# Optimization experiments

Measured on AMD Instinct MI355X. Metric: run time of the kernel, lower is better.

The kernel has to match this reference:

```python
import jax, jax.numpy as jnp
import numpy as np

E_LAMBDA = 1e-4


def _conv1d(x, w, b=None, pad=0):
    # x: (C, L) unbatched, w: (O, I, K)
    y = jax.lax.conv_general_dilated(
        x[None], w, window_strides=(1,), padding=[(pad, pad)],
        dimension_numbers=("NCH", "OIH", "NCH"))[0]
    if b is not None:
        y = y + b[:, None]
    return y


def _avg_pool2(x):
    # kernel 2 stride 2 along last axis; x: (C, L) -> (C, L//2)
    C, L = x.shape
    return x.reshape(C, L // 2, 2).mean(axis=-1)


def _simam(x):
    # x: (C, L); torch version runs on (1, C, L) so stats are global
    n = x.shape[0] * x.shape[1] - 1
    d = (x - x.mean()) ** 2
    y = d / (4.0 * (d.sum() / n + E_LAMBDA)) + 0.5
    return x + x * jax.nn.sigmoid(y)


def setup_inputs() -> dict:
    key = jax.random.key(0)
    ks = jax.random.split(key, 6)
    C, L = 2048, 4096  # L must equal 2*C for Tiss broadcast to be valid
    inp = jax.random.normal(ks[0], (C, L), dtype=jnp.float32)
    insum = jax.random.normal(ks[1], (C, L), dtype=jnp.float32)
    conv1_w = jax.random.normal(ks[2], (C, C, 3), dtype=jnp.float32) * (1.0 / np.sqrt(3 * C))
    fc_w = jax.random.normal(ks[3], (C, C, 1), dtype=jnp.float32) * (1.0 / np.sqrt(C))
    fc_b = jax.random.normal(ks[4], (C,), dtype=jnp.float32) * 0.01
    mix_w = jnp.array([-0.8], dtype=jnp.float32)
    return {"input": inp, "insum": insum, "conv1_w": conv1_w,
            "fc_w": fc_w, "fc_b": fc_b, "mix_w": mix_w}


def reference(input, insum, conv1_w, fc_w, fc_b, mix_w):
    x = _avg_pool2(input)        # (C, L/2)
    x_mfcc = _avg_pool2(insum)   # (C, L/2)

    input_new = _simam(input)
    insum_new = _simam(insum)

    x1 = _conv1d(x, conv1_w, pad=1)          # (C, L/2)
    x_mfcc1 = _conv1d(x_mfcc, conv1_w, pad=1)
    x2 = _conv1d(x, fc_w, fc_b, pad=0).T      # (L/2, C)
    x_mfcc2 = _conv1d(x_mfcc1, fc_w, fc_b, pad=0).T  # (L/2, C)

    out1 = jax.nn.sigmoid((x1 @ x_mfcc2).sum(axis=1))          # (C,)
    out2 = jax.nn.sigmoid((x_mfcc1.T @ x2.T).sum(axis=1))      # (L/2,) == (C,)

    mf = jax.nn.sigmoid(mix_w)                                  # (1,)
    out = out1 * mf + out2 * (1.0 - mf)                         # (C,)

    out = jax.nn.sigmoid(_conv1d(out[:, None], conv1_w, pad=1))  # (C, 1)

    input_insum = input_new * 0.6 + insum_new * 0.4             # (C, L)
    return input_insum * out
```

## Files before the change

### kernel.cpp

```cpp
#include <hip/hip_runtime.h>
#include <math.h>

#define C  2048
#define L  4096
#define L2 2048
#define CW3 6144

constexpr size_t OFF_RS_A = 0;
constexpr size_t OFF_RQ_A = 2048;
constexpr size_t OFF_RS_B = 4096;
constexpr size_t OFF_RQ_B = 6144;
constexpr size_t OFF_SCAL = 8192;
constexpr size_t OFF_CW   = 8208;
constexpr size_t OFF_G    = 10256;
constexpr size_t OFF_H    = 16400;
constexpr size_t OFF_V    = 22544;
constexpr size_t OFF_O2   = 24592;
constexpr size_t OFF_S    = 26640;
constexpr size_t OFF_U    = 28688;
constexpr size_t OFF_MIX  = 34832;

constexpr size_t PA_OFF = 0;
constexpr size_t PB_OFF = 4194304;

__device__ __forceinline__ float wredf(float v) {
#pragma unroll
  for (int o = 32; o; o >>= 1) v += __shfl_down(v, o, 64);
  return v;
}
__device__ __forceinline__ double wredd(double v) {
#pragma unroll
  for (int o = 32; o; o >>= 1) v += __shfl_down(v, o, 64);
  return v;
}
__device__ __forceinline__ float sigm(float x) { return 1.f / (1.f + expf(-x)); }
__device__ __forceinline__ float simam1(float x, float m, float cf) {
  float d = x - m;
  float y = d * d * cf + 0.5f;
  return x * (1.f + 1.f / (1.f + expf(-y)));
}

__global__ void w1(const float* __restrict__ A, const float* __restrict__ B,
                   const float* __restrict__ fc_w, float* __restrict__ ws,
                   float* __restrict__ dout) {
  int u = blockIdx.x;
  int tid = threadIdx.x;
  if (u < 4096) {
    __shared__ float sm[8];
    const float* src = (u < 2048) ? A : B;
    int row = u & 2047;
    const float4* p = (const float4*)(src + (size_t)row * L);
    float2* pool = (float2*)(dout + ((u < 2048) ? PA_OFF : PB_OFF) + (size_t)row * L2);
    float s = 0.f, q = 0.f;
#pragma unroll
    for (int i = tid; i < L / 4; i += 256) {
      float4 v = p[i];
      s += (v.x + v.y) + (v.z + v.w);
      q += (v.x * v.x + v.y * v.y) + (v.z * v.z + v.w * v.w);
      float2 pm;
      pm.x = (v.x + v.y) * 0.5f;
      pm.y = (v.z + v.w) * 0.5f;
      pool[i] = pm;
    }
    s = wredf(s); q = wredf(q);
    int lane = tid & 63, wv = tid >> 6;
    if (!lane) { sm[wv] = s; sm[4 + wv] = q; }
    __syncthreads();
    if (!tid) {
      float* rs = ws + ((u < 2048) ? OFF_RS_A : OFF_RS_B);
      float* rq = ws + ((u < 2048) ? OFF_RQ_A : OFF_RQ_B);
      rs[row] = sm[0] + sm[1] + sm[2] + sm[3];
      rq[row] = sm[4] + sm[5] + sm[6] + sm[7];
    }
  } else {
    int cb = u - 4096;
    int rg = cb >> 3;
    int col = (cb & 7) * 256 + tid;
    const float* p = fc_w + (size_t)rg * 64 * C + col;
    float acc = 0.f;
#pragma unroll 8
    for (int k = 0; k < 64; ++k) acc += p[(size_t)k * C];
    atomicAdd(ws + OFF_CW + col, acc);
  }
}

__global__ void w2(const float* __restrict__ fc_w, const float* __restrict__ fc_b,
                   float* __restrict__ ws) {
  int u = blockIdx.x;
  int tid = threadIdx.x;
  int lane = tid & 63, wv = tid >> 6;
  if (u < 2048) {
    __shared__ float sl[4];
    const float4* w = (const float4*)(fc_w + (size_t)u * C);
    const float4* rx = (const float4*)(ws + OFF_RS_A);
    float acc = 0.f;
#pragma unroll
    for (int i = tid; i < C / 4; i += 256) {
      float4 a = w[i], r = rx[i];
      acc += a.x * r.x + a.y * r.y + a.z * r.z + a.w * r.w;
    }
    acc = wredf(acc);
    if (!lane) sl[wv] = acc;
    __syncthreads();
    if (!tid)
      (ws + OFF_S)[u] = 0.5f * (sl[0] + sl[1] + sl[2] + sl[3]) + (float)L2 * fc_b[u];
  } else {
    __shared__ double sd[5];
    const float* arr = ws + (wv == 0 ? OFF_RS_A : wv == 1 ? OFF_RQ_A
                                                          : wv == 2 ? OFF_RS_B : OFF_RQ_B);
    double acc = 0.0, accb = 0.0;
    for (int i = lane; i < 2048; i += 64) {
      acc += (double)arr[i];
      if (wv == 0) accb += (double)fc_b[i];
    }
    acc = wredd(acc);
    if (wv == 0) accb = wredd(accb);
    if (!lane) { sd[wv] = acc; if (wv == 0) sd[4] = accb; }
    __syncthreads();
    if (!tid) {
      const double N = (double)C * (double)L, n = N - 1.0;
      double dA = sd[1] - sd[0] * sd[0] / N;
      double dB = sd[3] - sd[2] * sd[2] / N;
      float* s = ws + OFF_SCAL;
      s[0] = (float)(sd[0] / N);
      s[1] = (float)(1.0 / (4.0 * (dA / n + 1e-4)));
      s[2] = (float)(sd[2] / N);
      s[3] = (float)(1.0 / (4.0 * (dB / n + 1e-4)));
      s[4] = (float)sd[4];
    }
  }
}

__global__ void w3(const float* __restrict__ conv1_w, float* __restrict__ ws) {
  __shared__ float lcw[64], ls[64];
  int u = blockIdx.x;
  int tid = threadIdx.x;
  int cc = u % 24, rg = u / 24;
  int col = cc * 256 + tid;
  int i0 = rg * 64;
  if (tid < 64) {
    lcw[tid] = (ws + OFF_CW)[i0 + tid];
    ls[tid] = (ws + OFF_S)[i0 + tid];
  }
  __syncthreads();
  const float* base = conv1_w + (size_t)i0 * CW3 + col;
  float ag = 0.f, ah = 0.f;
#pragma unroll 8
  for (int k = 0; k < 64; ++k) {
    float wv = base[(size_t)k * CW3];
    ag += lcw[k] * wv;
    ah += ls[k] * wv;
  }
  atomicAdd(ws + OFF_G + col, ag);
  atomicAdd(ws + OFF_H + col, ah);
}

__global__ void w4(const float* __restrict__ dout, float* __restrict__ ws) {
  __shared__ float gsh[48], hsh[48];
  int u = blockIdx.x;
  int tid = threadIdx.x;
  int kb = u & 7, cg = u >> 3;
  int c0 = cg * 16;
  int k = kb * 256 + tid;
  if (tid < 48) gsh[tid] = (ws + OFF_G)[c0 * 3 + tid];
  else if (tid >= 64 && tid < 112) hsh[tid - 64] = (ws + OFF_H)[c0 * 3 + tid - 64];
  __syncthreads();
  float accv = 0.f, acco = 0.f;
#pragma unroll
  for (int c = 0; c < 16; ++c) {
    const float* row = dout + PB_OFF + (size_t)(c0 + c) * L2;
    float xc = row[k];
    float xl = (k > 0) ? row[k - 1] : 0.f;
    float xr = (k < L2 - 1) ? row[k + 1] : 0.f;
    accv += gsh[c * 3] * xl + gsh[c * 3 + 1] * xc + gsh[c * 3 + 2] * xr;
    acco += hsh[c * 3] * xl + hsh[c * 3 + 1] * xc + hsh[c * 3 + 2] * xr;
  }
  atomicAdd(ws + OFF_V + k, accv);
  atomicAdd(ws + OFF_O2 + k, acco);
}

__global__ void w5(const float* __restrict__ dout, float* __restrict__ ws) {
  __shared__ float vsh[2050];
  __shared__ float s12[12];
  int u = blockIdx.x;
  int tid = threadIdx.x;
  float sb = (ws + OFF_SCAL)[4];
  if (tid == 0) { vsh[0] = 0.f; vsh[2049] = 0.f; }
  for (int j = tid; j < L2; j += 256) vsh[1 + j] = (ws + OFF_V)[j] + sb;
  __syncthreads();
  const float* prow = dout + PA_OFF + (size_t)u * L2;
  float a0 = 0.f, a1 = 0.f, a2 = 0.f;
#pragma unroll
  for (int j = tid; j < L2; j += 256) {
    float xm = prow[j];
    a0 += xm * vsh[j + 2];
    a1 += xm * vsh[j + 1];
    a2 += xm * vsh[j];
  }
  a0 = wredf(a0); a1 = wredf(a1); a2 = wredf(a2);
  int lane = tid & 63, wv = tid >> 6;
  if (!lane) { s12[wv] = a0; s12[4 + wv] = a1; s12[8 + wv] = a2; }
  __syncthreads();
  if (!tid) {
    (ws + OFF_U)[u * 3 + 0] = s12[0] + s12[1] + s12[2] + s12[3];
    (ws + OFF_U)[u * 3 + 1] = s12[4] + s12[5] + s12[6] + s12[7];
    (ws + OFF_U)[u * 3 + 2] = s12[8] + s12[9] + s12[10] + s12[11];
  }
}

__global__ void w6(const float* __restrict__ conv1_w, const float* __restrict__ mix_w,
                   float* __restrict__ ws) {
  __shared__ float sl[4];
  int u = blockIdx.x;
  int tid = threadIdx.x;
  const float4* w4p = (const float4*)(conv1_w + (size_t)u * CW3);
  const float4* u4 = (const float4*)(ws + OFF_U);
  float acc = 0.f;
#pragma unroll
  for (int m = tid; m < CW3 / 4; m += 256) {
    float4 wv = w4p[m], uv = u4[m];
    acc += wv.x * uv.x + wv.y * uv.y + wv.z * uv.z + wv.w * uv.w;
  }
  acc = wredf(acc);
  int lane = tid & 63, wv = tid >> 6;
  if (!lane) sl[wv] = acc;
  __syncthreads();
  if (!tid) {
    float mfv = sigm(mix_w[0]);
    float o1 = sigm(sl[0] + sl[1] + sl[2] + sl[3]);
    float o2 = sigm((ws + OFF_O2)[u]);
    (ws + OFF_MIX)[u] = o1 * mfv + o2 * (1.f - mfv);
  }
}

__global__ void w7(const float* __restrict__ input, const float* __restrict__ insum,
                   const float* __restrict__ conv1_w, float* __restrict__ out,
                   const float* __restrict__ ws) {
  __shared__ float sl[4];
  __shared__ float shov;
  int u = blockIdx.x;
  int tid = threadIdx.x;
  const float4* w4p = (const float4*)(conv1_w + (size_t)u * CW3);
  const float4* m4 = (const float4*)(ws + OFF_MIX);
  float acc = 0.f;
#pragma unroll
  for (int p = tid; p < 512; p += 256) {
    float4 f0 = w4p[3 * p], f1 = w4p[3 * p + 1], f2 = w4p[3 * p + 2];
    float4 m = m4[p];
    acc += f0.y * m.x + f1.x * m.y + f1.w * m.z + f2.z * m.w;
  }
  acc = wredf(acc);
  int lane = tid & 63, wv = tid >> 6;
  if (!lane) sl[wv] = acc;
  __syncthreads();
  if (!tid) shov = sigm(sl[0] + sl[1] + sl[2] + sl[3]);
  __syncthreads();
  float ovc = shov;
  const float* scal = ws + OFF_SCAL;
  float mA = scal[0], cA = scal[1], mB = scal[2], cB = scal[3];
  size_t base = (size_t)u * L;
  const float4* pa = (const float4*)(input + base);
  const float4* pb = (const float4*)(insum + base);
  float4* po = (float4*)(out + base);
#pragma unroll
  for (int i = tid; i < L / 4; i += 256) {
    float4 a = pa[i], b = pb[i], r;
    r.x = (simam1(a.x, mA, cA) * 0.6f + simam1(b.x, mB, cB) * 0.4f) * ovc;
    r.y = (simam1(a.y, mA, cA) * 0.6f + simam1(b.y, mB, cB) * 0.4f) * ovc;
    r.z = (simam1(a.z, mA, cA) * 0.6f + simam1(b.z, mB, cB) * 0.4f) * ovc;
    r.w = (simam1(a.w, mA, cA) * 0.6f + simam1(b.w, mB, cB) * 0.4f) * ovc;
    po[i] = r;
  }
}

extern "C" void kernel_launch(void* const* d_in, const int* in_sizes, int n_in,
                              void* d_out, int out_size, void* d_ws, size_t ws_size,
                              hipStream_t stream) {
  const float* input   = (const float*)d_in[0];
  const float* insum   = (const float*)d_in[1];
  const float* conv1_w = (const float*)d_in[2];
  const float* fc_w    = (const float*)d_in[3];
  const float* fc_b    = (const float*)d_in[4];
  const float* mix_w   = (const float*)d_in[5];
  float* out = (float*)d_out;
  float* ws  = (float*)d_ws;

  hipMemsetAsync((char*)d_ws + OFF_CW * 4, 0, 18432 * 4, stream);

  dim3 b(256);
  w1<<<4352, b, 0, stream>>>(input, insum, fc_w, ws, out);
  w2<<<2049, b, 0, stream>>>(fc_w, fc_b, ws);
  w3<<<768, b, 0, stream>>>(conv1_w, ws);
  w4<<<1024, b, 0, stream>>>(out, ws);
  w5<<<2048, b, 0, stream>>>(out, ws);
  w6<<<2048, b, 0, stream>>>(conv1_w, mix_w, ws);
  w7<<<2048, b, 0, stream>>>(input, insum, conv1_w, out, ws);
}
```

Baseline: 235.0 us.

## Fuse all stages into one cooperative persistent kernel and recompute pooling on the fly

Merges the seven separate kernels into a single cooperative kernel that uses grid-wide syncs between stages and grid-stride loops over the original block indices. The intent is to remove launch overheads and gaps between kernels. It also stops writing the pooled intermediates to the output buffer and instead recomputes the avg-pool from the raw input and insum rows in the later stages, which drops a write and reread of that data. The costs are the grid.sync barriers, a fixed persistent grid size, and extra reads of the full-resolution rows in the stencil stage.

```diff
diff --git a/kernel.cpp b/kernel.cpp
--- a/kernel.cpp
+++ b/kernel.cpp
@@ -1,5 +1,8 @@
 #include <hip/hip_runtime.h>
+#include <hip/hip_cooperative_groups.h>
 #include <math.h>
+
+namespace cg = cooperative_groups;
 
 #define C  2048
 #define L  4096
@@ -20,9 +23,6 @@
 constexpr size_t OFF_U    = 28688;
 constexpr size_t OFF_MIX  = 34832;
 
-constexpr size_t PA_OFF = 0;
-constexpr size_t PB_OFF = 4194304;
-
 __device__ __forceinline__ float wredf(float v) {
 #pragma unroll
   for (int o = 32; o; o >>= 1) v += __shfl_down(v, o, 64);
@@ -40,236 +40,234 @@
   return x * (1.f + 1.f / (1.f + expf(-y)));
 }
 
-__global__ void w1(const float* __restrict__ A, const float* __restrict__ B,
-                   const float* __restrict__ fc_w, float* __restrict__ ws,
-                   float* __restrict__ dout) {
-  int u = blockIdx.x;
-  int tid = threadIdx.x;
-  if (u < 4096) {
-    __shared__ float sm[8];
-    const float* src = (u < 2048) ? A : B;
-    int row = u & 2047;
-    const float4* p = (const float4*)(src + (size_t)row * L);
-    float2* pool = (float2*)(dout + ((u < 2048) ? PA_OFF : PB_OFF) + (size_t)row * L2);
-    float s = 0.f, q = 0.f;
+__global__ __launch_bounds__(256, 4) void fused(
+    const float* __restrict__ input, const float* __restrict__ insum,
+    const float* __restrict__ conv1_w, const float* __restrict__ fc_w,
+    const float* __restrict__ fc_b, const float* __restrict__ mix_w,
+    float* __restrict__ out, float* __restrict__ ws) {
+  cg::grid_group grid = cg::this_grid();
+  const int tid = threadIdx.x;
+  const int lane = tid & 63, wv = tid >> 6;
+  const int nb = gridDim.x;
+  __shared__ float smem[2064];
+  __shared__ double sdsh[5];
+
+  for (int u = blockIdx.x; u < 4352; u += nb) {
+    if (u < 4096) {
+      const float* src = (u < 2048) ? input : insum;
+      int row = u & 2047;
+      const float4* p = (const float4*)(src + (size_t)row * L);
+      float s = 0.f, q = 0.f;
+#pragma unroll
+      for (int i = tid; i < L / 4; i += 256) {
+        float4 v = p[i];
+        s += (v.x + v.y) + (v.z + v.w);
+        q += (v.x * v.x + v.y * v.y) + (v.z * v.z + v.w * v.w);
+      }
+      s = wredf(s); q = wredf(q);
+      if (!lane) { smem[wv] = s; smem[4 + wv] = q; }
+      __syncthreads();
+      if (!tid) {
+        float* rs = ws + ((u < 2048) ? OFF_RS_A : OFF_RS_B);
+        float* rq = ws + ((u < 2048) ? OFF_RQ_A : OFF_RQ_B);
+        rs[row] = smem[0] + smem[1] + smem[2] + smem[3];
+        rq[row] = smem[4] + smem[5] + smem[6] + smem[7];
+      }
+      __syncthreads();
+    } else {
+      int cb = u - 4096;
+      int rg = cb >> 3;
+      int col = (cb & 7) * 256 + tid;
+      const float* p = fc_w + (size_t)rg * 64 * C + col;
+      float acc = 0.f;
+#pragma unroll 8
+      for (int k = 0; k < 64; ++k) acc += p[(size_t)k * C];
+      atomicAdd(ws + OFF_CW + col, acc);
+    }
+  }
+  grid.sync();
+
+  for (int u = blockIdx.x; u < 2049; u += nb) {
+    if (u < 2048) {
+      const float4* w = (const float4*)(fc_w + (size_t)u * C);
+      const float4* rx = (const float4*)(ws + OFF_RS_A);
+      float acc = 0.f;
+#pragma unroll
+      for (int i = tid; i < C / 4; i += 256) {
+        float4 a = w[i], r = rx[i];
+        acc += a.x * r.x + a.y * r.y + a.z * r.z + a.w * r.w;
+      }
+      acc = wredf(acc);
+      if (!lane) smem[wv] = acc;
+      __syncthreads();
+      if (!tid)
+        (ws + OFF_S)[u] = 0.5f * (smem[0] + smem[1] + smem[2] + smem[3]) + (float)L2 * fc_b[u];
+      __syncthreads();
+    } else {
+      const float* arr = ws + (wv == 0 ? OFF_RS_A : wv == 1 ? OFF_RQ_A
+                                                            : wv == 2 ? OFF_RS_B : OFF_RQ_B);
+      double acc = 0.0, accb = 0.0;
+      for (int i = lane; i < 2048; i += 64) {
+        acc += (double)arr[i];
+        if (wv == 0) accb += (double)fc_b[i];
+      }
+      acc = wredd(acc);
+      if (wv == 0) accb = wredd(accb);
+      if (!lane) { sdsh[wv] = acc; if (wv == 0) sdsh[4] = accb; }
+      __syncthreads();
+      if (!tid) {
+        const double N = (double)C * (double)L, n = N - 1.0;
+        double dA = sdsh[1] - sdsh[0] * sdsh[0] / N;
+        double dB = sdsh[3] - sdsh[2] * sdsh[2] / N;
+        float* sc = ws + OFF_SCAL;
+        sc[0] = (float)(sdsh[0] / N);
+        sc[1] = (float)(1.0 / (4.0 * (dA / n + 1e-4)));
+        sc[2] = (float)(sdsh[2] / N);
+        sc[3] = (float)(1.0 / (4.0 * (dB / n + 1e-4)));
+        sc[4] = (float)sdsh[4];
+      }
+      __syncthreads();
+    }
+  }
+  grid.sync();
+
+  for (int u = blockIdx.x; u < 768; u += nb) {
+    float* lcw = smem;
+    float* ls  = smem + 64;
+    int cc = u % 24, rg = u / 24;
+    int col = cc * 256 + tid;
+    int i0 = rg * 64;
+    if (tid < 64) {
+      lcw[tid] = (ws + OFF_CW)[i0 + tid];
+      ls[tid] = (ws + OFF_S)[i0 + tid];
+    }
+    __syncthreads();
+    const float* base = conv1_w + (size_t)i0 * CW3 + col;
+    float ag = 0.f, ah = 0.f;
+#pragma unroll 8
+    for (int k = 0; k < 64; ++k) {
+      float wvv = base[(size_t)k * CW3];
+      ag += lcw[k] * wvv;
+      ah += ls[k] * wvv;
+    }
+    atomicAdd(ws + OFF_G + col, ag);
+    atomicAdd(ws + OFF_H + col, ah);
+    __syncthreads();
+  }
+  grid.sync();
+
+  for (int u = blockIdx.x; u < 1024; u += nb) {
+    float* gsh = smem;
+    float* hsh = smem + 48;
+    int kb = u & 7, cgp = u >> 3;
+    int c0 = cgp * 16;
+    int k = kb * 256 + tid;
+    if (tid < 48) gsh[tid] = (ws + OFF_G)[c0 * 3 + tid];
+    else if (tid >= 64 && tid < 112) hsh[tid - 64] = (ws + OFF_H)[c0 * 3 + tid - 64];
+    __syncthreads();
+    float accv = 0.f, acco = 0.f;
+#pragma unroll
+    for (int c = 0; c < 16; ++c) {
+      const float* row = insum + (size_t)(c0 + c) * L;
+      float2 fm = *(const float2*)(row + 2 * k);
+      float xc = 0.5f * (fm.x + fm.y);
+      float xl = 0.f, xr = 0.f;
+      if (k > 0)      { float2 f = *(const float2*)(row + 2 * k - 2); xl = 0.5f * (f.x + f.y); }
+      if (k < L2 - 1) { float2 f = *(const float2*)(row + 2 * k + 2); xr = 0.5f * (f.x + f.y); }
+      accv += gsh[c * 3] * xl + gsh[c * 3 + 1] * xc + gsh[c * 3 + 2] * xr;
+      acco += hsh[c * 3] * xl + hsh[c * 3 + 1] * xc + hsh[c * 3 + 2] * xr;
+    }
+    atomicAdd(ws + OFF_V + k, accv);
+    atomicAdd(ws + OFF_O2 + k, acco);
+    __syncthreads();
+  }
+  grid.sync();
+
+  {
+    float sb = (ws + OFF_SCAL)[4];
+    if (tid == 0) { smem[0] = 0.f; smem[2049] = 0.f; }
+    for (int j = tid; j < L2; j += 256) smem[1 + j] = (ws + OFF_V)[j] + sb;
+    __syncthreads();
+    float* s12 = smem + 2050;
+    for (int u = blockIdx.x; u < 2048; u += nb) {
+      const float4* prow = (const float4*)(input + (size_t)u * L);
+      float a0 = 0.f, a1 = 0.f, a2 = 0.f;
+#pragma unroll
+      for (int i = tid; i < L / 4; i += 256) {
+        float4 f = prow[i];
+        float p0 = 0.5f * (f.x + f.y), p1 = 0.5f * (f.z + f.w);
+        int j = 2 * i;
+        a0 += p0 * smem[j + 2] + p1 * smem[j + 3];
+        a1 += p0 * smem[j + 1] + p1 * smem[j + 2];
+        a2 += p0 * smem[j]     + p1 * smem[j + 1];
+      }
+      a0 = wredf(a0); a1 = wredf(a1); a2 = wredf(a2);
+      if (!lane) { s12[wv] = a0; s12[4 + wv] = a1; s12[8 + wv] = a2; }
+      __syncthreads();
+      if (!tid) {
+        (ws + OFF_U)[u * 3 + 0] = s12[0] + s12[1] + s12[2] + s12[3];
+        (ws + OFF_U)[u * 3 + 1] = s12[4] + s12[5] + s12[6] + s12[7];
+        (ws + OFF_U)[u * 3 + 2] = s12[8] + s12[9] + s12[10] + s12[11];
+      }
+      __syncthreads();
+    }
+  }
+  grid.sync();
+
+  for (int u = blockIdx.x; u < 2048; u += nb) {
+    const float4* w4p = (const float4*)(conv1_w + (size_t)u * CW3);
+    const float4* u4 = (const float4*)(ws + OFF_U);
+    float acc = 0.f;
+#pragma unroll
+    for (int m = tid; m < CW3 / 4; m += 256) {
+      float4 wvv = w4p[m], uv = u4[m];
+      acc += wvv.x * uv.x + wvv.y * uv.y + wvv.z * uv.z + wvv.w * uv.w;
+    }
+    acc = wredf(acc);
+    if (!lane) smem[wv] = acc;
+    __syncthreads();
+    if (!tid) {
+      float mfv = sigm(mix_w[0]);
+      float o1 = sigm(smem[0] + smem[1] + smem[2] + smem[3]);
+      float o2 = sigm((ws + OFF_O2)[u]);
+      (ws + OFF_MIX)[u] = o1 * mfv + o2 * (1.f - mfv);
+    }
+    __syncthreads();
+  }
+  grid.sync();
+
+  for (int u = blockIdx.x; u < 2048; u += nb) {
+    const float4* w4p = (const float4*)(conv1_w + (size_t)u * CW3);
+    const float4* m4 = (const float4*)(ws + OFF_MIX);
+    float acc = 0.f;
+#pragma unroll
+    for (int p = tid; p < 512; p += 256) {
+      float4 f0 = w4p[3 * p], f1 = w4p[3 * p + 1], f2 = w4p[3 * p + 2];
+      float4 m = m4[p];
+      acc += f0.y * m.x + f1.x * m.y + f1.w * m.z + f2.z * m.w;
+    }
+    acc = wredf(acc);
+    if (!lane) smem[wv] = acc;
+    __syncthreads();
+    if (!tid) smem[8] = sigm(smem[0] + smem[1] + smem[2] + smem[3]);
+    __syncthreads();
+    float ovc = smem[8];
+    const float* scal = ws + OFF_SCAL;
+    float mA = scal[0], cA = scal[1], mB = scal[2], cB = scal[3];
+    size_t base = (size_t)u * L;
+    const float4* pa = (const float4*)(input + base);
+    const float4* pb = (const float4*)(insum + base);
+    float4* po = (float4*)(out + base);
 #pragma unroll
     for (int i = tid; i < L / 4; i += 256) {
-      float4 v = p[i];
-      s += (v.x + v.y) + (v.z + v.w);
-      q += (v.x * v.x + v.y * v.y) + (v.z * v.z + v.w * v.w);
-      float2 pm;
-      pm.x = (v.x + v.y) * 0.5f;
-      pm.y = (v.z + v.w) * 0.5f;
-      pool[i] = pm;
-    }
-    s = wredf(s); q = wredf(q);
-    int lane = tid & 63, wv = tid >> 6;
-    if (!lane) { sm[wv] = s; sm[4 + wv] = q; }
-    __syncthreads();
-    if (!tid) {
-      float* rs = ws + ((u < 2048) ? OFF_RS_A : OFF_RS_B);
-      float* rq = ws + ((u < 2048) ? OFF_RQ_A : OFF_RQ_B);
-      rs[row] = sm[0] + sm[1] + sm[2] + sm[3];
-      rq[row] = sm[4] + sm[5] + sm[6] + sm[7];
-    }
-  } else {
-    int cb = u - 4096;
-    int rg = cb >> 3;
-    int col = (cb & 7) * 256 + tid;
-    const float* p = fc_w + (size_t)rg * 64 * C + col;
-    float acc = 0.f;
-#pragma unroll 8
-    for (int k = 0; k < 64; ++k) acc += p[(size_t)k * C];
-    atomicAdd(ws + OFF_CW + col, acc);
-  }
-}
-
-__global__ void w2(const float* __restrict__ fc_w, const float* __restrict__ fc_b,
-                   float* __restrict__ ws) {
-  int u = blockIdx.x;
-  int tid = threadIdx.x;
-  int lane = tid & 63, wv = tid >> 6;
-  if (u < 2048) {
-    __shared__ float sl[4];
-    const float4* w = (const float4*)(fc_w + (size_t)u * C);
-    const float4* rx = (const float4*)(ws + OFF_RS_A);
-    float acc = 0.f;
-#pragma unroll
-    for (int i = tid; i < C / 4; i += 256) {
-      float4 a = w[i], r = rx[i];
-      acc += a.x * r.x + a.y * r.y + a.z * r.z + a.w * r.w;
-    }
-    acc = wredf(acc);
-    if (!lane) sl[wv] = acc;
-    __syncthreads();
-    if (!tid)
-      (ws + OFF_S)[u] = 0.5f * (sl[0] + sl[1] + sl[2] + sl[3]) + (float)L2 * fc_b[u];
-  } else {
-    __shared__ double sd[5];
-    const float* arr = ws + (wv == 0 ? OFF_RS_A : wv == 1 ? OFF_RQ_A
-                                                          : wv == 2 ? OFF_RS_B : OFF_RQ_B);
-    double acc = 0.0, accb = 0.0;
-    for (int i = lane; i < 2048; i += 64) {
-      acc += (double)arr[i];
-      if (wv == 0) accb += (double)fc_b[i];
-    }
-    acc = wredd(acc);
-    if (wv == 0) accb = wredd(accb);
-    if (!lane) { sd[wv] = acc; if (wv == 0) sd[4] = accb; }
-    __syncthreads();
-    if (!tid) {
-      const double N = (double)C * (double)L, n = N - 1.0;
-      double dA = sd[1] - sd[0] * sd[0] / N;
-      double dB = sd[3] - sd[2] * sd[2] / N;
-      float* s = ws + OFF_SCAL;
-      s[0] = (float)(sd[0] / N);
-      s[1] = (float)(1.0 / (4.0 * (dA / n + 1e-4)));
-      s[2] = (float)(sd[2] / N);
-      s[3] = (float)(1.0 / (4.0 * (dB / n + 1e-4)));
-      s[4] = (float)sd[4];
-    }
-  }
-}
-
-__global__ void w3(const float* __restrict__ conv1_w, float* __restrict__ ws) {
-  __shared__ float lcw[64], ls[64];
-  int u = blockIdx.x;
-  int tid = threadIdx.x;
-  int cc = u % 24, rg = u / 24;
-  int col = cc * 256 + tid;
-  int i0 = rg * 64;
-  if (tid < 64) {
-    lcw[tid] = (ws + OFF_CW)[i0 + tid];
-    ls[tid] = (ws + OFF_S)[i0 + tid];
-  }
-  __syncthreads();
-  const float* base = conv1_w + (size_t)i0 * CW3 + col;
-  float ag = 0.f, ah = 0.f;
-#pragma unroll 8
-  for (int k = 0; k < 64; ++k) {
-    float wv = base[(size_t)k * CW3];
-    ag += lcw[k] * wv;
-    ah += ls[k] * wv;
-  }
-  atomicAdd(ws + OFF_G + col, ag);
-  atomicAdd(ws + OFF_H + col, ah);
-}
-
-__global__ void w4(const float* __restrict__ dout, float* __restrict__ ws) {
-  __shared__ float gsh[48], hsh[48];
-  int u = blockIdx.x;
-  int tid = threadIdx.x;
-  int kb = u & 7, cg = u >> 3;
-  int c0 = cg * 16;
-  int k = kb * 256 + tid;
-  if (tid < 48) gsh[tid] = (ws + OFF_G)[c0 * 3 + tid];
-  else if (tid >= 64 && tid < 112) hsh[tid - 64] = (ws + OFF_H)[c0 * 3 + tid - 64];
-  __syncthreads();
-  float accv = 0.f, acco = 0.f;
-#pragma unroll
-  for (int c = 0; c < 16; ++c) {
-    const float* row = dout + PB_OFF + (size_t)(c0 + c) * L2;
-    float xc = row[k];
-    float xl = (k > 0) ? row[k - 1] : 0.f;
-    float xr = (k < L2 - 1) ? row[k + 1] : 0.f;
-    accv += gsh[c * 3] * xl + gsh[c * 3 + 1] * xc + gsh[c * 3 + 2] * xr;
-    acco += hsh[c * 3] * xl + hsh[c * 3 + 1] * xc + hsh[c * 3 + 2] * xr;
-  }
-  atomicAdd(ws + OFF_V + k, accv);
-  atomicAdd(ws + OFF_O2 + k, acco);
-}
-
-__global__ void w5(const float* __restrict__ dout, float* __restrict__ ws) {
-  __shared__ float vsh[2050];
-  __shared__ float s12[12];
-  int u = blockIdx.x;
-  int tid = threadIdx.x;
-  float sb = (ws + OFF_SCAL)[4];
-  if (tid == 0) { vsh[0] = 0.f; vsh[2049] = 0.f; }
-  for (int j = tid; j < L2; j += 256) vsh[1 + j] = (ws + OFF_V)[j] + sb;
-  __syncthreads();
-  const float* prow = dout + PA_OFF + (size_t)u * L2;
-  float a0 = 0.f, a1 = 0.f, a2 = 0.f;
-#pragma unroll
-  for (int j = tid; j < L2; j += 256) {
-    float xm = prow[j];
-    a0 += xm * vsh[j + 2];
-    a1 += xm * vsh[j + 1];
-    a2 += xm * vsh[j];
-  }
-  a0 = wredf(a0); a1 = wredf(a1); a2 = wredf(a2);
-  int lane = tid & 63, wv = tid >> 6;
-  if (!lane) { s12[wv] = a0; s12[4 + wv] = a1; s12[8 + wv] = a2; }
-  __syncthreads();
-  if (!tid) {
-    (ws + OFF_U)[u * 3 + 0] = s12[0] + s12[1] + s12[2] + s12[3];
-    (ws + OFF_U)[u * 3 + 1] = s12[4] + s12[5] + s12[6] + s12[7];
-    (ws + OFF_U)[u * 3 + 2] = s12[8] + s12[9] + s12[10] + s12[11];
-  }
-}
-
-__global__ void w6(const float* __restrict__ conv1_w, const float* __restrict__ mix_w,
-                   float* __restrict__ ws) {
-  __shared__ float sl[4];
-  int u = blockIdx.x;
-  int tid = threadIdx.x;
-  const float4* w4p = (const float4*)(conv1_w + (size_t)u * CW3);
-  const float4* u4 = (const float4*)(ws + OFF_U);
-  float acc = 0.f;
-#pragma unroll
-  for (int m = tid; m < CW3 / 4; m += 256) {
-    float4 wv = w4p[m], uv = u4[m];
-    acc += wv.x * uv.x + wv.y * uv.y + wv.z * uv.z + wv.w * uv.w;
-  }
-  acc = wredf(acc);
-  int lane = tid & 63, wv = tid >> 6;
-  if (!lane) sl[wv] = acc;
-  __syncthreads();
-  if (!tid) {
-    float mfv = sigm(mix_w[0]);
-    float o1 = sigm(sl[0] + sl[1] + sl[2] + sl[3]);
-    float o2 = sigm((ws + OFF_O2)[u]);
-    (ws + OFF_MIX)[u] = o1 * mfv + o2 * (1.f - mfv);
-  }
-}
-
-__global__ void w7(const float* __restrict__ input, const float* __restrict__ insum,
-                   const float* __restrict__ conv1_w, float* __restrict__ out,
-                   const float* __restrict__ ws) {
-  __shared__ float sl[4];
-  __shared__ float shov;
-  int u = blockIdx.x;
-  int tid = threadIdx.x;
-  const float4* w4p = (const float4*)(conv1_w + (size_t)u * CW3);
-  const float4* m4 = (const float4*)(ws + OFF_MIX);
-  float acc = 0.f;
-#pragma unroll
-  for (int p = tid; p < 512; p += 256) {
-    float4 f0 = w4p[3 * p], f1 = w4p[3 * p + 1], f2 = w4p[3 * p + 2];
-    float4 m = m4[p];
-    acc += f0.y * m.x + f1.x * m.y + f1.w * m.z + f2.z * m.w;
-  }
-  acc = wredf(acc);
-  int lane = tid & 63, wv = tid >> 6;
-  if (!lane) sl[wv] = acc;
-  __syncthreads();
-  if (!tid) shov = sigm(sl[0] + sl[1] + sl[2] + sl[3]);
-  __syncthreads();
-  float ovc = shov;
-  const float* scal = ws + OFF_SCAL;
-  float mA = scal[0], cA = scal[1], mB = scal[2], cB = scal[3];
-  size_t base = (size_t)u * L;
-  const float4* pa = (const float4*)(input + base);
-  const float4* pb = (const float4*)(insum + base);
-  float4* po = (float4*)(out + base);
-#pragma unroll
-  for (int i = tid; i < L / 4; i += 256) {
-    float4 a = pa[i], b = pb[i], r;
-    r.x = (simam1(a.x, mA, cA) * 0.6f + simam1(b.x, mB, cB) * 0.4f) * ovc;
-    r.y = (simam1(a.y, mA, cA) * 0.6f + simam1(b.y, mB, cB) * 0.4f) * ovc;
-    r.z = (simam1(a.z, mA, cA) * 0.6f + simam1(b.z, mB, cB) * 0.4f) * ovc;
-    r.w = (simam1(a.w, mA, cA) * 0.6f + simam1(b.w, mB, cB) * 0.4f) * ovc;
-    po[i] = r;
+      float4 a = pa[i], b = pb[i], r;
+      r.x = (simam1(a.x, mA, cA) * 0.6f + simam1(b.x, mB, cB) * 0.4f) * ovc;
+      r.y = (simam1(a.y, mA, cA) * 0.6f + simam1(b.y, mB, cB) * 0.4f) * ovc;
+      r.z = (simam1(a.z, mA, cA) * 0.6f + simam1(b.z, mB, cB) * 0.4f) * ovc;
+      r.w = (simam1(a.w, mA, cA) * 0.6f + simam1(b.w, mB, cB) * 0.4f) * ovc;
+      po[i] = r;
+    }
+    __syncthreads();
   }
 }
 
@@ -287,12 +285,17 @@
 
   hipMemsetAsync((char*)d_ws + OFF_CW * 4, 0, 18432 * 4, stream);
 
-  dim3 b(256);
-  w1<<<4352, b, 0, stream>>>(input, insum, fc_w, ws, out);
-  w2<<<2049, b, 0, stream>>>(fc_w, fc_b, ws);
-  w3<<<768, b, 0, stream>>>(conv1_w, ws);
-  w4<<<1024, b, 0, stream>>>(out, ws);
-  w5<<<2048, b, 0, stream>>>(out, ws);
-  w6<<<2048, b, 0, stream>>>(conv1_w, mix_w, ws);
-  w7<<<2048, b, 0, stream>>>(input, insum, conv1_w, out, ws);
-}
+  static int nb = 0;
+  if (nb == 0) {
+    int perCU = 0;
+    if (hipOccupancyMaxActiveBlocksPerMultiprocessor(&perCU, (const void*)fused, 256, 0) != hipSuccess ||
+        perCU < 1)
+      perCU = 4;
+    long t = (long)perCU * 256;
+    nb = (t > 2048) ? 2048 : (int)t;
+  }
+
+  void* args[] = {(void*)&input, (void*)&insum, (void*)&conv1_w, (void*)&fc_w,
+                  (void*)&fc_b, (void*)&mix_w, (void*)&out, (void*)&ws};
+  hipLaunchCooperativeKernel((const void*)fused, dim3(nb), dim3(256), args, 0, stream);
+}
```

After: 603.7 us. +156.9%, slower.

## Drop pooled intermediates, recompute pooling on the fly, replace atomics with partials

Applied to the files above, without the earlier changes.

Stops writing the avg-pooled copies of input and insum to the output buffer. The later kernels instead read the original rows and pool them inline, which removes a large write and reread of intermediate traffic. The atomic accumulations of the fc_w column sums and of the G/H vectors are replaced by per-group partial buffers, stored in the output scratch and reduced by the consumer kernels. k2 also computes four rows per block, and k3 uses float4 loads. In exchange, the consumers do extra reduction loops and some input rows are reread from memory.

```diff
diff --git a/kernel.cpp b/kernel.cpp
--- a/kernel.cpp
+++ b/kernel.cpp
@@ -11,17 +11,15 @@
 constexpr size_t OFF_RS_B = 4096;
 constexpr size_t OFF_RQ_B = 6144;
 constexpr size_t OFF_SCAL = 8192;
-constexpr size_t OFF_CW   = 8208;
-constexpr size_t OFF_G    = 10256;
-constexpr size_t OFF_H    = 16400;
-constexpr size_t OFF_V    = 22544;
-constexpr size_t OFF_O2   = 24592;
-constexpr size_t OFF_S    = 26640;
-constexpr size_t OFF_U    = 28688;
-constexpr size_t OFF_MIX  = 34832;
-
-constexpr size_t PA_OFF = 0;
-constexpr size_t PB_OFF = 4194304;
+constexpr size_t OFF_V    = 8208;
+constexpr size_t OFF_O2   = 10256;
+constexpr size_t OFF_S    = 12304;
+constexpr size_t OFF_U    = 14352;
+constexpr size_t OFF_MIX  = 20496;
+
+constexpr size_t CWP_OFF = 0;
+constexpr size_t GP_OFF  = 65536;
+constexpr size_t HP_OFF  = 458752;
 
 __device__ __forceinline__ float wredf(float v) {
 #pragma unroll
@@ -40,70 +38,74 @@
   return x * (1.f + 1.f / (1.f + expf(-y)));
 }
 
-__global__ void w1(const float* __restrict__ A, const float* __restrict__ B,
+__global__ void k1(const float* __restrict__ A, const float* __restrict__ B,
                    const float* __restrict__ fc_w, float* __restrict__ ws,
-                   float* __restrict__ dout) {
-  int u = blockIdx.x;
-  int tid = threadIdx.x;
-  if (u < 4096) {
-    __shared__ float sm[8];
-    const float* src = (u < 2048) ? A : B;
-    int row = u & 2047;
-    const float4* p = (const float4*)(src + (size_t)row * L);
-    float2* pool = (float2*)(dout + ((u < 2048) ? PA_OFF : PB_OFF) + (size_t)row * L2);
-    float s = 0.f, q = 0.f;
+                   float* __restrict__ scr) {
+  int u = blockIdx.x, tid = threadIdx.x;
+  if (u < 2048) {
+    __shared__ float sm[16];
+    const float4* pa = (const float4*)(A + (size_t)u * L);
+    const float4* pb = (const float4*)(B + (size_t)u * L);
+    float sa = 0.f, qa = 0.f, sb = 0.f, qb = 0.f;
 #pragma unroll
     for (int i = tid; i < L / 4; i += 256) {
-      float4 v = p[i];
-      s += (v.x + v.y) + (v.z + v.w);
-      q += (v.x * v.x + v.y * v.y) + (v.z * v.z + v.w * v.w);
-      float2 pm;
-      pm.x = (v.x + v.y) * 0.5f;
-      pm.y = (v.z + v.w) * 0.5f;
-      pool[i] = pm;
-    }
-    s = wredf(s); q = wredf(q);
+      float4 va = pa[i], vb = pb[i];
+      sa += (va.x + va.y) + (va.z + va.w);
+      qa += (va.x * va.x + va.y * va.y) + (va.z * va.z + va.w * va.w);
+      sb += (vb.x + vb.y) + (vb.z + vb.w);
+      qb += (vb.x * vb.x + vb.y * vb.y) + (vb.z * vb.z + vb.w * vb.w);
+    }
+    sa = wredf(sa); qa = wredf(qa); sb = wredf(sb); qb = wredf(qb);
     int lane = tid & 63, wv = tid >> 6;
-    if (!lane) { sm[wv] = s; sm[4 + wv] = q; }
+    if (!lane) { sm[wv] = sa; sm[4 + wv] = qa; sm[8 + wv] = sb; sm[12 + wv] = qb; }
     __syncthreads();
     if (!tid) {
-      float* rs = ws + ((u < 2048) ? OFF_RS_A : OFF_RS_B);
-      float* rq = ws + ((u < 2048) ? OFF_RQ_A : OFF_RQ_B);
-      rs[row] = sm[0] + sm[1] + sm[2] + sm[3];
-      rq[row] = sm[4] + sm[5] + sm[6] + sm[7];
+      ws[OFF_RS_A + u] = sm[0] + sm[1] + sm[2] + sm[3];
+      ws[OFF_RQ_A + u] = sm[4] + sm[5] + sm[6] + sm[7];
+      ws[OFF_RS_B + u] = sm[8] + sm[9] + sm[10] + sm[11];
+      ws[OFF_RQ_B + u] = sm[12] + sm[13] + sm[14] + sm[15];
     }
   } else {
-    int cb = u - 4096;
+    int cb = u - 2048;
     int rg = cb >> 3;
     int col = (cb & 7) * 256 + tid;
     const float* p = fc_w + (size_t)rg * 64 * C + col;
     float acc = 0.f;
 #pragma unroll 8
     for (int k = 0; k < 64; ++k) acc += p[(size_t)k * C];
-    atomicAdd(ws + OFF_CW + col, acc);
-  }
-}
-
-__global__ void w2(const float* __restrict__ fc_w, const float* __restrict__ fc_b,
+    scr[CWP_OFF + (size_t)rg * 2048 + col] = acc;
+  }
+}
+
+__global__ void k2(const float* __restrict__ fc_w, const float* __restrict__ fc_b,
                    float* __restrict__ ws) {
-  int u = blockIdx.x;
-  int tid = threadIdx.x;
+  int u = blockIdx.x, tid = threadIdx.x;
   int lane = tid & 63, wv = tid >> 6;
-  if (u < 2048) {
-    __shared__ float sl[4];
-    const float4* w = (const float4*)(fc_w + (size_t)u * C);
+  if (u < 512) {
+    __shared__ float sl[16];
+    int r0 = u * 4;
     const float4* rx = (const float4*)(ws + OFF_RS_A);
-    float acc = 0.f;
+    const float4* w4 = (const float4*)fc_w;
+    float a0 = 0.f, a1 = 0.f, a2 = 0.f, a3 = 0.f;
 #pragma unroll
     for (int i = tid; i < C / 4; i += 256) {
-      float4 a = w[i], r = rx[i];
-      acc += a.x * r.x + a.y * r.y + a.z * r.z + a.w * r.w;
-    }
-    acc = wredf(acc);
-    if (!lane) sl[wv] = acc;
+      float4 r = rx[i];
+      float4 w0 = w4[(size_t)(r0 + 0) * 512 + i];
+      float4 w1 = w4[(size_t)(r0 + 1) * 512 + i];
+      float4 w2 = w4[(size_t)(r0 + 2) * 512 + i];
+      float4 w3 = w4[(size_t)(r0 + 3) * 512 + i];
+      a0 += w0.x * r.x + w0.y * r.y + w0.z * r.z + w0.w * r.w;
+      a1 += w1.x * r.x + w1.y * r.y + w1.z * r.z + w1.w * r.w;
+      a2 += w2.x * r.x + w2.y * r.y + w2.z * r.z + w2.w * r.w;
+      a3 += w3.x * r.x + w3.y * r.y + w3.z * r.z + w3.w * r.w;
+    }
+    a0 = wredf(a0); a1 = wredf(a1); a2 = wredf(a2); a3 = wredf(a3);
+    if (!lane) { sl[wv] = a0; sl[4 + wv] = a1; sl[8 + wv] = a2; sl[12 + wv] = a3; }
     __syncthreads();
-    if (!tid)
-      (ws + OFF_S)[u] = 0.5f * (sl[0] + sl[1] + sl[2] + sl[3]) + (float)L2 * fc_b[u];
+    if (tid < 4) {
+      float s_ = sl[tid * 4 + 0] + sl[tid * 4 + 1] + sl[tid * 4 + 2] + sl[tid * 4 + 3];
+      ws[OFF_S + r0 + tid] = 0.5f * s_ + (float)L2 * fc_b[r0 + tid];
+    }
   } else {
     __shared__ double sd[5];
     const float* arr = ws + (wv == 0 ? OFF_RS_A : wv == 1 ? OFF_RQ_A
@@ -121,81 +123,94 @@
       const double N = (double)C * (double)L, n = N - 1.0;
       double dA = sd[1] - sd[0] * sd[0] / N;
       double dB = sd[3] - sd[2] * sd[2] / N;
-      float* s = ws + OFF_SCAL;
-      s[0] = (float)(sd[0] / N);
-      s[1] = (float)(1.0 / (4.0 * (dA / n + 1e-4)));
-      s[2] = (float)(sd[2] / N);
-      s[3] = (float)(1.0 / (4.0 * (dB / n + 1e-4)));
-      s[4] = (float)sd[4];
-    }
-  }
-}
-
-__global__ void w3(const float* __restrict__ conv1_w, float* __restrict__ ws) {
-  __shared__ float lcw[64], ls[64];
-  int u = blockIdx.x;
-  int tid = threadIdx.x;
-  int cc = u % 24, rg = u / 24;
-  int col = cc * 256 + tid;
-  int i0 = rg * 64;
-  if (tid < 64) {
-    lcw[tid] = (ws + OFF_CW)[i0 + tid];
-    ls[tid] = (ws + OFF_S)[i0 + tid];
-  }
-  __syncthreads();
-  const float* base = conv1_w + (size_t)i0 * CW3 + col;
-  float ag = 0.f, ah = 0.f;
-#pragma unroll 8
-  for (int k = 0; k < 64; ++k) {
-    float wv = base[(size_t)k * CW3];
-    ag += lcw[k] * wv;
-    ah += ls[k] * wv;
-  }
-  atomicAdd(ws + OFF_G + col, ag);
-  atomicAdd(ws + OFF_H + col, ah);
-}
-
-__global__ void w4(const float* __restrict__ dout, float* __restrict__ ws) {
-  __shared__ float gsh[48], hsh[48];
-  int u = blockIdx.x;
-  int tid = threadIdx.x;
+      float* sc = ws + OFF_SCAL;
+      sc[0] = (float)(sd[0] / N);
+      sc[1] = (float)(1.0 / (4.0 * (dA / n + 1e-4)));
+      sc[2] = (float)(sd[2] / N);
+      sc[3] = (float)(1.0 / (4.0 * (dB / n + 1e-4)));
+      sc[4] = (float)sd[4];
+    }
+  }
+}
+
+__global__ void k3(const float* __restrict__ conv1_w, const float* __restrict__ ws,
+                   float* __restrict__ scr) {
+  __shared__ float lcw[32], ls[32];
+  int u = blockIdx.x, tid = threadIdx.x;
+  int rg = u / 6, cc = u % 6;
+  int i0 = rg * 32;
+  int col4 = cc * 256 + tid;
+  if (tid < 32) {
+    float a = 0.f;
+#pragma unroll 8
+    for (int g = 0; g < 32; ++g) a += scr[CWP_OFF + (size_t)g * 2048 + i0 + tid];
+    lcw[tid] = a;
+    ls[tid] = ws[OFF_S + i0 + tid];
+  }
+  __syncthreads();
+  const float4* cv = (const float4*)conv1_w;
+  float4 g4 = {0.f, 0.f, 0.f, 0.f}, h4 = {0.f, 0.f, 0.f, 0.f};
+#pragma unroll 8
+  for (int k = 0; k < 32; ++k) {
+    float4 w = cv[(size_t)(i0 + k) * 1536 + col4];
+    float cwv = lcw[k], sv = ls[k];
+    g4.x += cwv * w.x; g4.y += cwv * w.y; g4.z += cwv * w.z; g4.w += cwv * w.w;
+    h4.x += sv * w.x;  h4.y += sv * w.y;  h4.z += sv * w.z;  h4.w += sv * w.w;
+  }
+  ((float4*)(scr + GP_OFF + (size_t)rg * 6144))[col4] = g4;
+  ((float4*)(scr + HP_OFF + (size_t)rg * 6144))[col4] = h4;
+}
+
+__global__ void k4(const float* __restrict__ insum, const float* __restrict__ scr,
+                   float* __restrict__ ws) {
+  __shared__ float gs[96], hs[96];
+  int u = blockIdx.x, tid = threadIdx.x;
   int kb = u & 7, cg = u >> 3;
-  int c0 = cg * 16;
+  int c0 = cg * 32;
   int k = kb * 256 + tid;
-  if (tid < 48) gsh[tid] = (ws + OFF_G)[c0 * 3 + tid];
-  else if (tid >= 64 && tid < 112) hsh[tid - 64] = (ws + OFF_H)[c0 * 3 + tid - 64];
+  if (tid < 192) {
+    int t = (tid < 96) ? tid : tid - 96;
+    const float* base = scr + ((tid < 96) ? GP_OFF : HP_OFF) + (size_t)c0 * 3 + t;
+    float a = 0.f;
+#pragma unroll 8
+    for (int g = 0; g < 64; ++g) a += base[(size_t)g * 6144];
+    if (tid < 96) gs[t] = a; else hs[t] = a;
+  }
   __syncthreads();
   float accv = 0.f, acco = 0.f;
-#pragma unroll
-  for (int c = 0; c < 16; ++c) {
-    const float* row = dout + PB_OFF + (size_t)(c0 + c) * L2;
-    float xc = row[k];
-    float xl = (k > 0) ? row[k - 1] : 0.f;
-    float xr = (k < L2 - 1) ? row[k + 1] : 0.f;
-    accv += gsh[c * 3] * xl + gsh[c * 3 + 1] * xc + gsh[c * 3 + 2] * xr;
-    acco += hsh[c * 3] * xl + hsh[c * 3 + 1] * xc + hsh[c * 3 + 2] * xr;
+#pragma unroll 8
+  for (int c = 0; c < 32; ++c) {
+    const float* row = insum + (size_t)(c0 + c) * L;
+    float2 fm = *(const float2*)(row + 2 * k);
+    float xc = 0.5f * (fm.x + fm.y);
+    float xl = 0.f, xr = 0.f;
+    if (k > 0)      { float2 f = *(const float2*)(row + 2 * k - 2); xl = 0.5f * (f.x + f.y); }
+    if (k < L2 - 1) { float2 f = *(const float2*)(row + 2 * k + 2); xr = 0.5f * (f.x + f.y); }
+    accv += gs[c * 3] * xl + gs[c * 3 + 1] * xc + gs[c * 3 + 2] * xr;
+    acco += hs[c * 3] * xl + hs[c * 3 + 1] * xc + hs[c * 3 + 2] * xr;
   }
   atomicAdd(ws + OFF_V + k, accv);
   atomicAdd(ws + OFF_O2 + k, acco);
 }
 
-__global__ void w5(const float* __restrict__ dout, float* __restrict__ ws) {
+__global__ void k5(const float* __restrict__ input, float* __restrict__ ws) {
   __shared__ float vsh[2050];
   __shared__ float s12[12];
-  int u = blockIdx.x;
-  int tid = threadIdx.x;
+  int u = blockIdx.x, tid = threadIdx.x;
   float sb = (ws + OFF_SCAL)[4];
   if (tid == 0) { vsh[0] = 0.f; vsh[2049] = 0.f; }
   for (int j = tid; j < L2; j += 256) vsh[1 + j] = (ws + OFF_V)[j] + sb;
   __syncthreads();
-  const float* prow = dout + PA_OFF + (size_t)u * L2;
+  const float4* prow = (const float4*)(input + (size_t)u * L);
   float a0 = 0.f, a1 = 0.f, a2 = 0.f;
 #pragma unroll
-  for (int j = tid; j < L2; j += 256) {
-    float xm = prow[j];
-    a0 += xm * vsh[j + 2];
-    a1 += xm * vsh[j + 1];
-    a2 += xm * vsh[j];
+  for (int i = tid; i < L / 4; i += 256) {
+    float4 f = prow[i];
+    float p0 = 0.5f * (f.x + f.y), p1 = 0.5f * (f.z + f.w);
+    int j = 2 * i;
+    a0 += p0 * vsh[j + 2] + p1 * vsh[j + 3];
+    a1 += p0 * vsh[j + 1] + p1 * vsh[j + 2];
+    a2 += p0 * vsh[j]     + p1 * vsh[j + 1];
   }
   a0 = wredf(a0); a1 = wredf(a1); a2 = wredf(a2);
   int lane = tid & 63, wv = tid >> 6;
@@ -208,11 +223,10 @@
   }
 }
 
-__global__ void w6(const float* __restrict__ conv1_w, const float* __restrict__ mix_w,
+__global__ void k6(const float* __restrict__ conv1_w, const float* __restrict__ mix_w,
                    float* __restrict__ ws) {
   __shared__ float sl[4];
-  int u = blockIdx.x;
-  int tid = threadIdx.x;
+  int u = blockIdx.x, tid = threadIdx.x;
   const float4* w4p = (const float4*)(conv1_w + (size_t)u * CW3);
   const float4* u4 = (const float4*)(ws + OFF_U);
   float acc = 0.f;
@@ -233,13 +247,12 @@
   }
 }
 
-__global__ void w7(const float* __restrict__ input, const float* __restrict__ insum,
+__global__ void k7(const float* __restrict__ input, const float* __restrict__ insum,
                    const float* __restrict__ conv1_w, float* __restrict__ out,
                    const float* __restrict__ ws) {
   __shared__ float sl[4];
   __shared__ float shov;
-  int u = blockIdx.x;
-  int tid = threadIdx.x;
+  int u = blockIdx.x, tid = threadIdx.x;
   const float4* w4p = (const float4*)(conv1_w + (size_t)u * CW3);
   const float4* m4 = (const float4*)(ws + OFF_MIX);
   float acc = 0.f;
@@ -285,14 +298,14 @@
   float* out = (float*)d_out;
   float* ws  = (float*)d_ws;
 
-  hipMemsetAsync((char*)d_ws + OFF_CW * 4, 0, 18432 * 4, stream);
+  hipMemsetAsync((char*)d_ws + OFF_V * 4, 0, 4096 * 4, stream);
 
   dim3 b(256);
-  w1<<<4352, b, 0, stream>>>(input, insum, fc_w, ws, out);
-  w2<<<2049, b, 0, stream>>>(fc_w, fc_b, ws);
-  w3<<<768, b, 0, stream>>>(conv1_w, ws);
-  w4<<<1024, b, 0, stream>>>(out, ws);
-  w5<<<2048, b, 0, stream>>>(out, ws);
-  w6<<<2048, b, 0, stream>>>(conv1_w, mix_w, ws);
-  w7<<<2048, b, 0, stream>>>(input, insum, conv1_w, out, ws);
-}
+  k1<<<2304, b, 0, stream>>>(input, insum, fc_w, ws, out);
+  k2<<<513, b, 0, stream>>>(fc_w, fc_b, ws);
+  k3<<<384, b, 0, stream>>>(conv1_w, ws, out);
+  k4<<<512, b, 0, stream>>>(insum, out, ws);
+  k5<<<2048, b, 0, stream>>>(input, ws);
+  k6<<<2048, b, 0, stream>>>(conv1_w, mix_w, ws);
+  k7<<<2048, b, 0, stream>>>(input, insum, conv1_w, out, ws);
+}
```

Measured after the change: 246.8 us. +5.0%, slower.
